# Kernel tuning notes

Hardware: AMD Instinct MI355X
Metric: run time of the kernel (lower is better)

## Reference

```python
import jax, jax.numpy as jnp
import numpy as np

B, S, H, D = 256, 512, 512, 1  # batch, seq_len, rnn_hid_size (== S*D), input_dim


def lstm_cell(x, h, c, Wih, Whh, bih, bhh):
    # torch.nn.LSTMCell: gates ordered i, f, g, o
    g = x @ Wih.T + bih + h @ Whh.T + bhh  # [B, 4H]
    i, f, gg, o = jnp.split(g, 4, axis=-1)
    i = jax.nn.sigmoid(i)
    f = jax.nn.sigmoid(f)
    gg = jnp.tanh(gg)
    o = jax.nn.sigmoid(o)
    c_new = f * c + i * gg
    h_new = o * jnp.tanh(c_new)
    return h_new, c_new


def setup_inputs() -> dict:
    key = jax.random.key(0)
    ks = jax.random.split(key, 14)
    sc = 1.0 / np.sqrt(H)  # torch LSTMCell/Linear default uniform bound
    u = lambda k, shape: jax.random.uniform(k, shape, jnp.float32, -sc, sc)
    values = jax.random.normal(ks[0], (B, S), jnp.float32)
    masks = jax.random.randint(ks[1], (B, S), 0, 2).astype(jnp.float32)
    return {
        "values": values,
        "masks": masks,
        "Wih_f": u(ks[2], (4 * H, D)), "Whh_f": u(ks[3], (4 * H, H)),
        "bih_f": u(ks[4], (4 * H,)), "bhh_f": u(ks[5], (4 * H,)),
        "Wih_b": u(ks[6], (4 * H, D)), "Whh_b": u(ks[7], (4 * H, H)),
        "bih_b": u(ks[8], (4 * H,)), "bhh_b": u(ks[9], (4 * H,)),
        "W_imp": u(ks[10], (D, H)), "b_imp": u(ks[11], (D,)),
    }


def reference(values, masks, Wih_f, Whh_f, bih_f, bhh_f,
              Wih_b, Whh_b, bih_b, bhh_b, W_imp, b_imp):
    x_f = values[:, :, None]  # [B, S, 1]
    m_f = masks[:, :, None]
    # flip over axis 2 (size 1) is a no-op, matching the original exactly
    x_b = jnp.flip(x_f, axis=2)
    m_b = jnp.flip(m_f, axis=2)

    start_f = jnp.full((B, D), 128.0, jnp.float32)
    start_b = jnp.full((B, D), -128.0, jnp.float32)
    z = jnp.zeros((B, H), jnp.float32)
    h_f, c_f = lstm_cell(start_f, z, z, Wih_f, Whh_f, bih_f, bhh_f)
    h_b, c_b = lstm_cell(start_b, z, z, Wih_b, Whh_b, bih_b, bhh_b)

    xs = (jnp.swapaxes(x_f, 0, 1), jnp.swapaxes(m_f, 0, 1),
          jnp.swapaxes(x_b, 0, 1), jnp.swapaxes(m_b, 0, 1))  # [S, B, 1] each

    def step(carry, inp):
        hf, cf, hb, cb = carry
        xf, mf, xb, mb = inp
        imp_f = hf @ W_imp.T + b_imp
        imp_b = hb @ W_imp.T + b_imp
        cc_f = (1.0 - mf) * xf + mf * imp_f
        cc_b = (1.0 - mb) * xb + mb * imp_b
        hf, cf = lstm_cell(cc_f, hf, cf, Wih_f, Whh_f, bih_f, bhh_f)
        hb, cb = lstm_cell(cc_b, hb, cb, Wih_b, Whh_b, bih_b, bhh_b)
        return (hf, cf, hb, cb), None

    (h_f, c_f, h_b, c_b), _ = jax.lax.scan(step, (h_f, c_f, h_b, c_b), xs)
    h = h_f + h_b  # [B, H]
    imputations = h.reshape(B, S, D)  # requires H == S * D
    out = imputations * (1.0 - m_f) + x_f * m_f
    return h, out
```

## Files before the change

### kernel.cpp

```cpp
#include <hip/hip_runtime.h>
#include <stdint.h>

#define B_ 256
#define S_ 512
#define H_ 512

#define XM_STRIDE 513
#define LDS_BYTES 56320

typedef __attribute__((ext_vector_type(4))) float f32x4;
typedef __attribute__((ext_vector_type(4))) int   i32x4;
typedef __attribute__((ext_vector_type(8))) short s16x8;

__device__ __forceinline__ short f2bf(float f) {
    union { float f; uint32_t u; } c; c.f = f;
    uint32_t u = c.u;
    u += 0x7fffu + ((u >> 16) & 1u);
    return (short)(u >> 16);
}
__device__ __forceinline__ float bflo(uint32_t u) { return __builtin_bit_cast(float, u << 16); }
__device__ __forceinline__ float bfhi(uint32_t u) { return __builtin_bit_cast(float, u & 0xffff0000u); }
__device__ __forceinline__ float sig_(float x)  { return 1.0f / (1.0f + __expf(-x)); }
__device__ __forceinline__ float tanh_(float x) { return 1.0f - 2.0f / (1.0f + __expf(2.0f * x)); }

__device__ __forceinline__ void load_a16_issue(const void* p, i32x4* a) {
    asm volatile(
        "global_load_dwordx4 %0, %16, off sc0 sc1\n\t"
        "global_load_dwordx4 %1, %16, off offset:64 sc0 sc1\n\t"
        "global_load_dwordx4 %2, %16, off offset:128 sc0 sc1\n\t"
        "global_load_dwordx4 %3, %16, off offset:192 sc0 sc1\n\t"
        "global_load_dwordx4 %4, %16, off offset:256 sc0 sc1\n\t"
        "global_load_dwordx4 %5, %16, off offset:320 sc0 sc1\n\t"
        "global_load_dwordx4 %6, %16, off offset:384 sc0 sc1\n\t"
        "global_load_dwordx4 %7, %16, off offset:448 sc0 sc1\n\t"
        "global_load_dwordx4 %8, %16, off offset:512 sc0 sc1\n\t"
        "global_load_dwordx4 %9, %16, off offset:576 sc0 sc1\n\t"
        "global_load_dwordx4 %10, %16, off offset:640 sc0 sc1\n\t"
        "global_load_dwordx4 %11, %16, off offset:704 sc0 sc1\n\t"
        "global_load_dwordx4 %12, %16, off offset:768 sc0 sc1\n\t"
        "global_load_dwordx4 %13, %16, off offset:832 sc0 sc1\n\t"
        "global_load_dwordx4 %14, %16, off offset:896 sc0 sc1\n\t"
        "global_load_dwordx4 %15, %16, off offset:960 sc0 sc1"
        : "=v"(a[0]), "=v"(a[1]), "=v"(a[2]), "=v"(a[3]),
          "=v"(a[4]), "=v"(a[5]), "=v"(a[6]), "=v"(a[7]),
          "=v"(a[8]), "=v"(a[9]), "=v"(a[10]), "=v"(a[11]),
          "=v"(a[12]), "=v"(a[13]), "=v"(a[14]), "=v"(a[15])
        : "v"(p)
        : "memory");
}
#define AWAIT(imm, x0, x1, x2, x3) \
    asm volatile("s_waitcnt vmcnt(" #imm ")" : "+v"(x0), "+v"(x1), "+v"(x2), "+v"(x3) :: "memory")

__device__ __forceinline__ void store_h4(void* p, int h0, int h1, int h2, int h3) {
    asm volatile(
        "global_store_short %4, %0, off sc0 sc1\n\t"
        "global_store_short %4, %1, off offset:1024 sc0 sc1\n\t"
        "global_store_short %4, %2, off offset:2048 sc0 sc1\n\t"
        "global_store_short %4, %3, off offset:3072 sc0 sc1"
        :: "v"(h0), "v"(h1), "v"(h2), "v"(h3), "v"(p)
        : "memory");
}

__global__ void __launch_bounds__(128, 1)
lstm_kernel(const float* __restrict__ values, const float* __restrict__ masks,
            const float* __restrict__ Wih_f, const float* __restrict__ Whh_f,
            const float* __restrict__ bih_f, const float* __restrict__ bhh_f,
            const float* __restrict__ Wih_b, const float* __restrict__ Whh_b,
            const float* __restrict__ bih_b, const float* __restrict__ bhh_b,
            const float* __restrict__ W_imp, const float* __restrict__ b_imp,
            unsigned int* ctrs, short* h_buf, float* hfin)
{
    extern __shared__ char smem_raw[];
    short*    imp_lds = (short*)smem_raw;
    uint32_t* xm_lds  = (uint32_t*)(smem_raw + 16384);

    uint32_t* flags = (uint32_t*)ctrs + 64;

    const int tid  = threadIdx.x;
    const int lane = tid & 63;
    const int wave = tid >> 6;
    const int nw = wave;

    const int bid = blockIdx.x;
    const int g   = bid & 15;
    const int w   = (bid >> 4) & 15;
    const int d   = bid >> 8;
    const int cluster = d * 16 + g;

    const float* Whh = d ? Whh_b : Whh_f;
    const float* Wih = d ? Wih_b : Wih_f;
    const float* bih = d ? bih_b : bih_f;
    const float* bhh = d ? bhh_b : bhh_f;

    const int col16 = lane & 15;
    const int koff4 = lane >> 4;
    const int jcol  = w * 32 + nw * 16 + col16;

    for (int c = tid; c < 1024; c += 128) {
        int ckoff = (c >> 4) & 3, ckb = c >> 6;
        int k0 = ckb * 32 + ckoff * 8;
        short* dst = &imp_lds[c * 8];
        #pragma unroll
        for (int j = 0; j < 8; ++j) dst[j] = f2bf(W_imp[k0 + j]);
    }
    for (int i = tid; i < 16 * 512; i += 128) {
        int r = i >> 9, s = i & 511;
        float x = values[(g * 16 + r) * S_ + s];
        float m = masks[(g * 16 + r) * S_ + s];
        float a = x * (1.0f - m);
        xm_lds[r * XM_STRIDE + s] =
            (uint32_t)(uint16_t)f2bf(a) | ((uint32_t)(uint16_t)f2bf(m) << 16);
    }

    s16x8 bfr[4][16];
    {
        const float* base = Whh + (size_t)jcol * 512 + koff4 * 8;
        #pragma unroll
        for (int gg = 0; gg < 4; ++gg) {
            const float* src = base + (size_t)gg * 512 * 512;
            #pragma unroll
            for (int kb = 0; kb < 16; ++kb) {
                f32x4 v0 = *(const f32x4*)(src + kb * 32);
                f32x4 v1 = *(const f32x4*)(src + kb * 32 + 4);
                s16x8 b;
                b[0] = f2bf(v0[0]); b[1] = f2bf(v0[1]); b[2] = f2bf(v0[2]); b[3] = f2bf(v0[3]);
                b[4] = f2bf(v1[0]); b[5] = f2bf(v1[1]); b[6] = f2bf(v1[2]); b[7] = f2bf(v1[3]);
                bfr[gg][kb] = b;
            }
        }
    }

    float bias[4], wih[4];
    #pragma unroll
    for (int gg = 0; gg < 4; ++gg) {
        int gc = gg * 512 + jcol;
        bias[gg] = bih[gc] + bhh[gc];
        wih[gg]  = Wih[gc];
    }
    const float bimp  = b_imp[0];
    const float start = d ? -128.0f : 128.0f;

    const int arow    = g * 16 + col16;
    const int rowloc  = koff4 * 4;
    const int rowbase = g * 16 + rowloc;
    const int imp_off = (koff4 * 16 + col16) * 8;

    uint32_t*       myflag = flags + cluster * 16 + w;
    const uint32_t* pollp  = flags + cluster * 16 + col16;

    __syncthreads();

    float c_reg[4];
    {
        float pre[4];
        #pragma unroll
        for (int gg = 0; gg < 4; ++gg) pre[gg] = start * wih[gg] + bias[gg];
        float i0 = sig_(pre[0]), g0 = tanh_(pre[2]), o0 = sig_(pre[3]);
        float c0 = i0 * g0;
        float h0 = o0 * tanh_(c0);
        #pragma unroll
        for (int r = 0; r < 4; ++r) c_reg[r] = c0;
        int hb16 = (int)(unsigned short)(unsigned)f2bf(h0);
        short* dst = h_buf + d * (B_ * H_) + (size_t)rowbase * H_ + jcol;
        store_h4(dst, hb16, hb16, hb16, hb16);
    }
    asm volatile("s_waitcnt vmcnt(0)" ::: "memory");
    __syncthreads();
    if (tid == 0)
        asm volatile("global_store_dword %0, %1, off sc0 sc1" :: "v"(myflag), "v"(1u) : "memory");

    for (int t = 0; t < S_; ++t) {
        const int p = t & 1;
        const short* hb_r = h_buf + p       * (2 * B_ * H_) + d * (B_ * H_);
        short*       hb_w = h_buf + (p ^ 1) * (2 * B_ * H_) + d * (B_ * H_);

        if (wave == 0) {
            const uint32_t tgt = (uint32_t)(t + 1);
            for (;;) {
                uint32_t f;
                asm volatile("global_load_dword %0, %1, off sc0 sc1\n\ts_waitcnt vmcnt(0)"
                             : "=v"(f) : "v"(pollp) : "memory");
                if (__ballot(f >= tgt) == ~0ull) break;
                __builtin_amdgcn_s_sleep(2);
            }
        }
        __syncthreads();

        i32x4 a_regs[16];
        load_a16_issue(hb_r + (size_t)arow * H_ + koff4 * 8, a_regs);

        f32x4 acc0 = {0,0,0,0}, acc1 = {0,0,0,0}, acc2 = {0,0,0,0}, acc3 = {0,0,0,0};
        f32x4 acc4 = {0,0,0,0};
        AWAIT(12, a_regs[0], a_regs[1], a_regs[2], a_regs[3]);
        #pragma unroll
        for (int kb = 0; kb < 4; ++kb) {
            s16x8 a = __builtin_bit_cast(s16x8, a_regs[kb]);
            acc0 = __builtin_amdgcn_mfma_f32_16x16x32_bf16(a, bfr[0][kb], acc0, 0, 0, 0);
            acc1 = __builtin_amdgcn_mfma_f32_16x16x32_bf16(a, bfr[1][kb], acc1, 0, 0, 0);
            acc2 = __builtin_amdgcn_mfma_f32_16x16x32_bf16(a, bfr[2][kb], acc2, 0, 0, 0);
            acc3 = __builtin_amdgcn_mfma_f32_16x16x32_bf16(a, bfr[3][kb], acc3, 0, 0, 0);
            s16x8 b4 = *(const s16x8*)&imp_lds[kb * 512 + imp_off];
            acc4 = __builtin_amdgcn_mfma_f32_16x16x32_bf16(a, b4, acc4, 0, 0, 0);
        }
        AWAIT(8, a_regs[4], a_regs[5], a_regs[6], a_regs[7]);
        #pragma unroll
        for (int kb = 4; kb < 8; ++kb) {
            s16x8 a = __builtin_bit_cast(s16x8, a_regs[kb]);
            acc0 = __builtin_amdgcn_mfma_f32_16x16x32_bf16(a, bfr[0][kb], acc0, 0, 0, 0);
            acc1 = __builtin_amdgcn_mfma_f32_16x16x32_bf16(a, bfr[1][kb], acc1, 0, 0, 0);
            acc2 = __builtin_amdgcn_mfma_f32_16x16x32_bf16(a, bfr[2][kb], acc2, 0, 0, 0);
            acc3 = __builtin_amdgcn_mfma_f32_16x16x32_bf16(a, bfr[3][kb], acc3, 0, 0, 0);
            s16x8 b4 = *(const s16x8*)&imp_lds[kb * 512 + imp_off];
            acc4 = __builtin_amdgcn_mfma_f32_16x16x32_bf16(a, b4, acc4, 0, 0, 0);
        }
        AWAIT(4, a_regs[8], a_regs[9], a_regs[10], a_regs[11]);
        #pragma unroll
        for (int kb = 8; kb < 12; ++kb) {
            s16x8 a = __builtin_bit_cast(s16x8, a_regs[kb]);
            acc0 = __builtin_amdgcn_mfma_f32_16x16x32_bf16(a, bfr[0][kb], acc0, 0, 0, 0);
            acc1 = __builtin_amdgcn_mfma_f32_16x16x32_bf16(a, bfr[1][kb], acc1, 0, 0, 0);
            acc2 = __builtin_amdgcn_mfma_f32_16x16x32_bf16(a, bfr[2][kb], acc2, 0, 0, 0);
            acc3 = __builtin_amdgcn_mfma_f32_16x16x32_bf16(a, bfr[3][kb], acc3, 0, 0, 0);
            s16x8 b4 = *(const s16x8*)&imp_lds[kb * 512 + imp_off];
            acc4 = __builtin_amdgcn_mfma_f32_16x16x32_bf16(a, b4, acc4, 0, 0, 0);
        }
        AWAIT(0, a_regs[12], a_regs[13], a_regs[14], a_regs[15]);
        #pragma unroll
        for (int kb = 12; kb < 16; ++kb) {
            s16x8 a = __builtin_bit_cast(s16x8, a_regs[kb]);
            acc0 = __builtin_amdgcn_mfma_f32_16x16x32_bf16(a, bfr[0][kb], acc0, 0, 0, 0);
            acc1 = __builtin_amdgcn_mfma_f32_16x16x32_bf16(a, bfr[1][kb], acc1, 0, 0, 0);
            acc2 = __builtin_amdgcn_mfma_f32_16x16x32_bf16(a, bfr[2][kb], acc2, 0, 0, 0);
            acc3 = __builtin_amdgcn_mfma_f32_16x16x32_bf16(a, bfr[3][kb], acc3, 0, 0, 0);
            s16x8 b4 = *(const s16x8*)&imp_lds[kb * 512 + imp_off];
            acc4 = __builtin_amdgcn_mfma_f32_16x16x32_bf16(a, b4, acc4, 0, 0, 0);
        }

        int hbits[4];
        #pragma unroll
        for (int r = 0; r < 4; ++r) {
            uint32_t pk = xm_lds[(rowloc + r) * XM_STRIDE + t];
            float cc = bflo(pk) + bfhi(pk) * (acc4[r] + bimp);
            float pi = acc0[r] + cc * wih[0] + bias[0];
            float pf = acc1[r] + cc * wih[1] + bias[1];
            float pg = acc2[r] + cc * wih[2] + bias[2];
            float po = acc3[r] + cc * wih[3] + bias[3];
            float iv = sig_(pi), fv = sig_(pf), gv = tanh_(pg), ov = sig_(po);
            c_reg[r] = fv * c_reg[r] + iv * gv;
            float hn = ov * tanh_(c_reg[r]);
            hbits[r] = (int)(unsigned short)(unsigned)f2bf(hn);
            if (t == S_ - 1) hfin[d * (B_ * H_) + (rowbase + r) * H_ + jcol] = hn;
        }
        store_h4(hb_w + (size_t)rowbase * H_ + jcol, hbits[0], hbits[1], hbits[2], hbits[3]);

        asm volatile("s_waitcnt vmcnt(0)" ::: "memory");
        __syncthreads();
        if (tid == 0)
            asm volatile("global_store_dword %0, %1, off sc0 sc1"
                         :: "v"(myflag), "v"((uint32_t)(t + 2)) : "memory");
    }
}

__global__ void __launch_bounds__(256)
epilogue_kernel(const float* __restrict__ values, const float* __restrict__ masks,
                const float* __restrict__ hfin, float* __restrict__ out)
{
    int i = blockIdx.x * 256 + threadIdx.x;
    float h = hfin[i] + hfin[B_ * H_ + i];
    out[i] = h;
    float xv = values[i], mv = masks[i];
    out[B_ * H_ + i] = h * (1.0f - mv) + xv * mv;
}

extern "C" void kernel_launch(void* const* d_in, const int* in_sizes, int n_in,
                              void* d_out, int out_size, void* d_ws, size_t ws_size,
                              hipStream_t stream) {
    const float* values = (const float*)d_in[0];
    const float* masks  = (const float*)d_in[1];
    const float* Wih_f  = (const float*)d_in[2];
    const float* Whh_f  = (const float*)d_in[3];
    const float* bih_f  = (const float*)d_in[4];
    const float* bhh_f  = (const float*)d_in[5];
    const float* Wih_b  = (const float*)d_in[6];
    const float* Whh_b  = (const float*)d_in[7];
    const float* bih_b  = (const float*)d_in[8];
    const float* bhh_b  = (const float*)d_in[9];
    const float* W_imp  = (const float*)d_in[10];
    const float* b_imp  = (const float*)d_in[11];

    unsigned int* ctrs = (unsigned int*)d_ws;
    short* h_buf = (short*)((char*)d_ws + 8192);
    float* hfin  = (float*)((char*)d_ws + 8192 + 2 * 2 * B_ * H_ * sizeof(short));

    hipMemsetAsync(d_ws, 0, 8192, stream);

    hipFuncSetAttribute((const void*)lstm_kernel,
                        hipFuncAttributeMaxDynamicSharedMemorySize, LDS_BYTES);

    void* args[] = {
        (void*)&values, (void*)&masks,
        (void*)&Wih_f, (void*)&Whh_f, (void*)&bih_f, (void*)&bhh_f,
        (void*)&Wih_b, (void*)&Whh_b, (void*)&bih_b, (void*)&bhh_b,
        (void*)&W_imp, (void*)&b_imp,
        (void*)&ctrs, (void*)&h_buf, (void*)&hfin
    };
    hipError_t err = hipLaunchCooperativeKernel((const void*)lstm_kernel,
                                                dim3(512), dim3(128), args,
                                                (unsigned int)LDS_BYTES, stream);
    if (err != hipSuccess) {
        lstm_kernel<<<dim3(512), dim3(128), LDS_BYTES, stream>>>(
            values, masks, Wih_f, Whh_f, bih_f, bhh_f,
            Wih_b, Whh_b, bih_b, bhh_b, W_imp, b_imp, ctrs, h_buf, hfin);
    }

    epilogue_kernel<<<dim3((B_ * H_) / 256), dim3(256), 0, stream>>>(
        values, masks, hfin, (float*)d_out);
}
```

Measured before the change: 2.309 ms.

## Replace flag-based inter-block sync with sentinel polling on a 4-deep h ring

Drops the per-step flag counters, block barriers and store fences. Each block now polls the hidden-state data itself, retrying the load until no lane sees the 0xAAAA sentinel, and resets a stale ring slot back to the sentinel after each step. This is meant to remove one global round trip plus barrier latency from every recurrent step. It also writes the final h straight into the output buffer instead of a scratch buffer. Risks: repeated full-tile reloads while polling add memory traffic, the staged waits that overlapped loads with MFMA are gone, and a genuine bf16 value equal to the sentinel would stall the loop.

```diff
diff --git a/kernel.cpp b/kernel.cpp
--- a/kernel.cpp
+++ b/kernel.cpp
@@ -7,6 +7,8 @@
 
 #define XM_STRIDE 513
 #define LDS_BYTES 56320
+
+#define SENT ((int)0xAAAAAAAA)
 
 typedef __attribute__((ext_vector_type(4))) float f32x4;
 typedef __attribute__((ext_vector_type(4))) int   i32x4;
@@ -23,7 +25,7 @@
 __device__ __forceinline__ float sig_(float x)  { return 1.0f / (1.0f + __expf(-x)); }
 __device__ __forceinline__ float tanh_(float x) { return 1.0f - 2.0f / (1.0f + __expf(2.0f * x)); }
 
-__device__ __forceinline__ void load_a16_issue(const void* p, i32x4* a) {
+__device__ __forceinline__ void load_a16(const void* p, i32x4* a) {
     asm volatile(
         "global_load_dwordx4 %0, %16, off sc0 sc1\n\t"
         "global_load_dwordx4 %1, %16, off offset:64 sc0 sc1\n\t"
@@ -40,7 +42,8 @@
         "global_load_dwordx4 %12, %16, off offset:768 sc0 sc1\n\t"
         "global_load_dwordx4 %13, %16, off offset:832 sc0 sc1\n\t"
         "global_load_dwordx4 %14, %16, off offset:896 sc0 sc1\n\t"
-        "global_load_dwordx4 %15, %16, off offset:960 sc0 sc1"
+        "global_load_dwordx4 %15, %16, off offset:960 sc0 sc1\n\t"
+        "s_waitcnt vmcnt(0)"
         : "=v"(a[0]), "=v"(a[1]), "=v"(a[2]), "=v"(a[3]),
           "=v"(a[4]), "=v"(a[5]), "=v"(a[6]), "=v"(a[7]),
           "=v"(a[8]), "=v"(a[9]), "=v"(a[10]), "=v"(a[11]),
@@ -48,8 +51,6 @@
         : "v"(p)
         : "memory");
 }
-#define AWAIT(imm, x0, x1, x2, x3) \
-    asm volatile("s_waitcnt vmcnt(" #imm ")" : "+v"(x0), "+v"(x1), "+v"(x2), "+v"(x3) :: "memory")
 
 __device__ __forceinline__ void store_h4(void* p, int h0, int h1, int h2, int h3) {
     asm volatile(
@@ -68,24 +69,21 @@
             const float* __restrict__ Wih_b, const float* __restrict__ Whh_b,
             const float* __restrict__ bih_b, const float* __restrict__ bhh_b,
             const float* __restrict__ W_imp, const float* __restrict__ b_imp,
-            unsigned int* ctrs, short* h_buf, float* hfin)
+            short* h_buf, float* outbuf)
 {
     extern __shared__ char smem_raw[];
     short*    imp_lds = (short*)smem_raw;
     uint32_t* xm_lds  = (uint32_t*)(smem_raw + 16384);
 
-    uint32_t* flags = (uint32_t*)ctrs + 64;
-
     const int tid  = threadIdx.x;
     const int lane = tid & 63;
-    const int wave = tid >> 6;
-    const int nw = wave;
+    const int nw   = tid >> 6;
 
     const int bid = blockIdx.x;
     const int g   = bid & 15;
     const int w   = (bid >> 4) & 15;
     const int d   = bid >> 8;
-    const int cluster = d * 16 + g;
+    const int dofs = d * (B_ * H_);
 
     const float* Whh = d ? Whh_b : Whh_f;
     const float* Wih = d ? Wih_b : Wih_f;
@@ -145,9 +143,6 @@
     const int rowbase = g * 16 + rowloc;
     const int imp_off = (koff4 * 16 + col16) * 8;
 
-    uint32_t*       myflag = flags + cluster * 16 + w;
-    const uint32_t* pollp  = flags + cluster * 16 + col16;
-
     __syncthreads();
 
     float c_reg[4];
@@ -161,72 +156,36 @@
         #pragma unroll
         for (int r = 0; r < 4; ++r) c_reg[r] = c0;
         int hb16 = (int)(unsigned short)(unsigned)f2bf(h0);
-        short* dst = h_buf + d * (B_ * H_) + (size_t)rowbase * H_ + jcol;
-        store_h4(dst, hb16, hb16, hb16, hb16);
-    }
-    asm volatile("s_waitcnt vmcnt(0)" ::: "memory");
-    __syncthreads();
-    if (tid == 0)
-        asm volatile("global_store_dword %0, %1, off sc0 sc1" :: "v"(myflag), "v"(1u) : "memory");
-
+        store_h4(h_buf + dofs + (size_t)rowbase * H_ + jcol, hb16, hb16, hb16, hb16);
+    }
+
+    const size_t lane_off = (size_t)rowbase * H_ + jcol;
+    const size_t aoff     = (size_t)arow * H_ + koff4 * 8;
     for (int t = 0; t < S_; ++t) {
-        const int p = t & 1;
-        const short* hb_r = h_buf + p       * (2 * B_ * H_) + d * (B_ * H_);
-        short*       hb_w = h_buf + (p ^ 1) * (2 * B_ * H_) + d * (B_ * H_);
-
-        if (wave == 0) {
-            const uint32_t tgt = (uint32_t)(t + 1);
+        const short* rbuf = h_buf + ((t)     & 3) * (2 * B_ * H_) + dofs;
+        short*       wbuf = h_buf + ((t + 1) & 3) * (2 * B_ * H_) + dofs;
+        short*       sbuf = h_buf + ((t + 3) & 3) * (2 * B_ * H_) + dofs;
+
+        i32x4 a_regs[16];
+        {
+            const void* ap = rbuf + aoff;
             for (;;) {
-                uint32_t f;
-                asm volatile("global_load_dword %0, %1, off sc0 sc1\n\ts_waitcnt vmcnt(0)"
-                             : "=v"(f) : "v"(pollp) : "memory");
-                if (__ballot(f >= tgt) == ~0ull) break;
-                __builtin_amdgcn_s_sleep(2);
+                load_a16(ap, a_regs);
+                int bad = 0;
+                #pragma unroll
+                for (int j = 0; j < 16; ++j) {
+                    i32x4 v = a_regs[j];
+                    bad |= (v[0] == SENT) | (v[1] == SENT) | (v[2] == SENT) | (v[3] == SENT);
+                }
+                if (__ballot(bad != 0) == 0ull) break;
+                __builtin_amdgcn_s_sleep(1);
             }
         }
-        __syncthreads();
-
-        i32x4 a_regs[16];
-        load_a16_issue(hb_r + (size_t)arow * H_ + koff4 * 8, a_regs);
 
         f32x4 acc0 = {0,0,0,0}, acc1 = {0,0,0,0}, acc2 = {0,0,0,0}, acc3 = {0,0,0,0};
         f32x4 acc4 = {0,0,0,0};
-        AWAIT(12, a_regs[0], a_regs[1], a_regs[2], a_regs[3]);
-        #pragma unroll
-        for (int kb = 0; kb < 4; ++kb) {
-            s16x8 a = __builtin_bit_cast(s16x8, a_regs[kb]);
-            acc0 = __builtin_amdgcn_mfma_f32_16x16x32_bf16(a, bfr[0][kb], acc0, 0, 0, 0);
-            acc1 = __builtin_amdgcn_mfma_f32_16x16x32_bf16(a, bfr[1][kb], acc1, 0, 0, 0);
-            acc2 = __builtin_amdgcn_mfma_f32_16x16x32_bf16(a, bfr[2][kb], acc2, 0, 0, 0);
-            acc3 = __builtin_amdgcn_mfma_f32_16x16x32_bf16(a, bfr[3][kb], acc3, 0, 0, 0);
-            s16x8 b4 = *(const s16x8*)&imp_lds[kb * 512 + imp_off];
-            acc4 = __builtin_amdgcn_mfma_f32_16x16x32_bf16(a, b4, acc4, 0, 0, 0);
-        }
-        AWAIT(8, a_regs[4], a_regs[5], a_regs[6], a_regs[7]);
-        #pragma unroll
-        for (int kb = 4; kb < 8; ++kb) {
-            s16x8 a = __builtin_bit_cast(s16x8, a_regs[kb]);
-            acc0 = __builtin_amdgcn_mfma_f32_16x16x32_bf16(a, bfr[0][kb], acc0, 0, 0, 0);
-            acc1 = __builtin_amdgcn_mfma_f32_16x16x32_bf16(a, bfr[1][kb], acc1, 0, 0, 0);
-            acc2 = __builtin_amdgcn_mfma_f32_16x16x32_bf16(a, bfr[2][kb], acc2, 0, 0, 0);
-            acc3 = __builtin_amdgcn_mfma_f32_16x16x32_bf16(a, bfr[3][kb], acc3, 0, 0, 0);
-            s16x8 b4 = *(const s16x8*)&imp_lds[kb * 512 + imp_off];
-            acc4 = __builtin_amdgcn_mfma_f32_16x16x32_bf16(a, b4, acc4, 0, 0, 0);
-        }
-        AWAIT(4, a_regs[8], a_regs[9], a_regs[10], a_regs[11]);
-        #pragma unroll
-        for (int kb = 8; kb < 12; ++kb) {
-            s16x8 a = __builtin_bit_cast(s16x8, a_regs[kb]);
-            acc0 = __builtin_amdgcn_mfma_f32_16x16x32_bf16(a, bfr[0][kb], acc0, 0, 0, 0);
-            acc1 = __builtin_amdgcn_mfma_f32_16x16x32_bf16(a, bfr[1][kb], acc1, 0, 0, 0);
-            acc2 = __builtin_amdgcn_mfma_f32_16x16x32_bf16(a, bfr[2][kb], acc2, 0, 0, 0);
-            acc3 = __builtin_amdgcn_mfma_f32_16x16x32_bf16(a, bfr[3][kb], acc3, 0, 0, 0);
-            s16x8 b4 = *(const s16x8*)&imp_lds[kb * 512 + imp_off];
-            acc4 = __builtin_amdgcn_mfma_f32_16x16x32_bf16(a, b4, acc4, 0, 0, 0);
-        }
-        AWAIT(0, a_regs[12], a_regs[13], a_regs[14], a_regs[15]);
-        #pragma unroll
-        for (int kb = 12; kb < 16; ++kb) {
+        #pragma unroll
+        for (int kb = 0; kb < 16; ++kb) {
             s16x8 a = __builtin_bit_cast(s16x8, a_regs[kb]);
             acc0 = __builtin_amdgcn_mfma_f32_16x16x32_bf16(a, bfr[0][kb], acc0, 0, 0, 0);
             acc1 = __builtin_amdgcn_mfma_f32_16x16x32_bf16(a, bfr[1][kb], acc1, 0, 0, 0);
@@ -249,24 +208,20 @@
             c_reg[r] = fv * c_reg[r] + iv * gv;
             float hn = ov * tanh_(c_reg[r]);
             hbits[r] = (int)(unsigned short)(unsigned)f2bf(hn);
-            if (t == S_ - 1) hfin[d * (B_ * H_) + (rowbase + r) * H_ + jcol] = hn;
-        }
-        store_h4(hb_w + (size_t)rowbase * H_ + jcol, hbits[0], hbits[1], hbits[2], hbits[3]);
-
-        asm volatile("s_waitcnt vmcnt(0)" ::: "memory");
-        __syncthreads();
-        if (tid == 0)
-            asm volatile("global_store_dword %0, %1, off sc0 sc1"
-                         :: "v"(myflag), "v"((uint32_t)(t + 2)) : "memory");
+            if (t == S_ - 1) outbuf[dofs + lane_off + (size_t)r * H_] = hn;
+        }
+        store_h4(wbuf + lane_off, hbits[0], hbits[1], hbits[2], hbits[3]);
+        store_h4(sbuf + lane_off, 0xAAAA, 0xAAAA, 0xAAAA, 0xAAAA);
     }
 }
 
 __global__ void __launch_bounds__(256)
 epilogue_kernel(const float* __restrict__ values, const float* __restrict__ masks,
-                const float* __restrict__ hfin, float* __restrict__ out)
+                float* __restrict__ out)
 {
     int i = blockIdx.x * 256 + threadIdx.x;
-    float h = hfin[i] + hfin[B_ * H_ + i];
+    float hf = out[i], hb = out[B_ * H_ + i];
+    float h = hf + hb;
     out[i] = h;
     float xv = values[i], mv = masks[i];
     out[B_ * H_ + i] = h * (1.0f - mv) + xv * mv;
@@ -288,11 +243,10 @@
     const float* W_imp  = (const float*)d_in[10];
     const float* b_imp  = (const float*)d_in[11];
 
-    unsigned int* ctrs = (unsigned int*)d_ws;
-    short* h_buf = (short*)((char*)d_ws + 8192);
-    float* hfin  = (float*)((char*)d_ws + 8192 + 2 * 2 * B_ * H_ * sizeof(short));
-
-    hipMemsetAsync(d_ws, 0, 8192, stream);
+    short* h_buf = (short*)d_ws;
+    hipMemsetAsync(d_ws, 0xAA, 4 * 2 * B_ * H_ * sizeof(short), stream);
+
+    float* outbuf = (float*)d_out;
 
     hipFuncSetAttribute((const void*)lstm_kernel,
                         hipFuncAttributeMaxDynamicSharedMemorySize, LDS_BYTES);
@@ -302,7 +256,7 @@
         (void*)&Wih_f, (void*)&Whh_f, (void*)&bih_f, (void*)&bhh_f,
         (void*)&Wih_b, (void*)&Whh_b, (void*)&bih_b, (void*)&bhh_b,
         (void*)&W_imp, (void*)&b_imp,
-        (void*)&ctrs, (void*)&h_buf, (void*)&hfin
+        (void*)&h_buf, (void*)&outbuf
     };
     hipError_t err = hipLaunchCooperativeKernel((const void*)lstm_kernel,
                                                 dim3(512), dim3(128), args,
@@ -310,9 +264,9 @@
     if (err != hipSuccess) {
         lstm_kernel<<<dim3(512), dim3(128), LDS_BYTES, stream>>>(
             values, masks, Wih_f, Whh_f, bih_f, bhh_f,
-            Wih_b, Whh_b, bih_b, bhh_b, W_imp, b_imp, ctrs, h_buf, hfin);
+            Wih_b, Whh_b, bih_b, bhh_b, W_imp, b_imp, h_buf, outbuf);
     }
 
     epilogue_kernel<<<dim3((B_ * H_) / 256), dim3(256), 0, stream>>>(
-        values, masks, hfin, (float*)d_out);
-}
+        values, masks, outbuf);
+}
```

After: 4.910 ms. 113% more time.

## Use per-wave step flags and LDS-transposed coalesced hidden-state stores

Applied to the files above, without the earlier changes.

Each wave now publishes its own step-completion flag, so the block-wide barrier before signalling is gone. Consumers poll 32 flags per cluster instead of 16, which needs a larger flag region and memset. The scattered 2-byte global stores of h are replaced by a small per-wave LDS transpose followed by one dwordx2 store per lane, and the spin-wait sleep is shortened. The aim is lower per-timestep latency on the serial recurrence, paid for with more flag polling traffic and an extra LDS round trip.

```diff
diff --git a/kernel.cpp b/kernel.cpp
--- a/kernel.cpp
+++ b/kernel.cpp
@@ -10,6 +10,7 @@
 
 typedef __attribute__((ext_vector_type(4))) float f32x4;
 typedef __attribute__((ext_vector_type(4))) int   i32x4;
+typedef __attribute__((ext_vector_type(2))) int   i32x2;
 typedef __attribute__((ext_vector_type(8))) short s16x8;
 
 __device__ __forceinline__ short f2bf(float f) {
@@ -73,13 +74,13 @@
     extern __shared__ char smem_raw[];
     short*    imp_lds = (short*)smem_raw;
     uint32_t* xm_lds  = (uint32_t*)(smem_raw + 16384);
+    short*    tr_lds  = (short*)(smem_raw + 49216);
 
     uint32_t* flags = (uint32_t*)ctrs + 64;
 
     const int tid  = threadIdx.x;
     const int lane = tid & 63;
-    const int wave = tid >> 6;
-    const int nw = wave;
+    const int nw   = tid >> 6;
 
     const int bid = blockIdx.x;
     const int g   = bid & 15;
@@ -145,8 +146,12 @@
     const int rowbase = g * 16 + rowloc;
     const int imp_off = (koff4 * 16 + col16) * 8;
 
-    uint32_t*       myflag = flags + cluster * 16 + w;
-    const uint32_t* pollp  = flags + cluster * 16 + col16;
+    uint32_t*       myflag = flags + cluster * 64 + w * 2 + nw;
+    const uint32_t* pollp  = flags + cluster * 64 + (lane & 31);
+
+    short* trw = tr_lds + nw * 320;
+    const int row16 = lane & 15;
+    const int half  = lane >> 4;
 
     __syncthreads();
 
@@ -161,12 +166,10 @@
         #pragma unroll
         for (int r = 0; r < 4; ++r) c_reg[r] = c0;
         int hb16 = (int)(unsigned short)(unsigned)f2bf(h0);
-        short* dst = h_buf + d * (B_ * H_) + (size_t)rowbase * H_ + jcol;
-        store_h4(dst, hb16, hb16, hb16, hb16);
+        store_h4(h_buf + d * (B_ * H_) + (size_t)rowbase * H_ + jcol, hb16, hb16, hb16, hb16);
     }
     asm volatile("s_waitcnt vmcnt(0)" ::: "memory");
-    __syncthreads();
-    if (tid == 0)
+    if (lane == 0)
         asm volatile("global_store_dword %0, %1, off sc0 sc1" :: "v"(myflag), "v"(1u) : "memory");
 
     for (int t = 0; t < S_; ++t) {
@@ -174,14 +177,14 @@
         const short* hb_r = h_buf + p       * (2 * B_ * H_) + d * (B_ * H_);
         short*       hb_w = h_buf + (p ^ 1) * (2 * B_ * H_) + d * (B_ * H_);
 
-        if (wave == 0) {
+        if (nw == 0) {
             const uint32_t tgt = (uint32_t)(t + 1);
             for (;;) {
                 uint32_t f;
                 asm volatile("global_load_dword %0, %1, off sc0 sc1\n\ts_waitcnt vmcnt(0)"
                              : "=v"(f) : "v"(pollp) : "memory");
                 if (__ballot(f >= tgt) == ~0ull) break;
-                __builtin_amdgcn_s_sleep(2);
+                __builtin_amdgcn_s_sleep(1);
             }
         }
         __syncthreads();
@@ -249,13 +252,20 @@
             c_reg[r] = fv * c_reg[r] + iv * gv;
             float hn = ov * tanh_(c_reg[r]);
             hbits[r] = (int)(unsigned short)(unsigned)f2bf(hn);
-            if (t == S_ - 1) hfin[d * (B_ * H_) + (rowbase + r) * H_ + jcol] = hn;
-        }
-        store_h4(hb_w + (size_t)rowbase * H_ + jcol, hbits[0], hbits[1], hbits[2], hbits[3]);
+            if (t == S_ - 1)
+                hfin[d * (B_ * H_) + (size_t)(rowbase + r) * H_ + jcol] = hn;
+        }
+
+        #pragma unroll
+        for (int r = 0; r < 4; ++r)
+            trw[(rowloc + r) * 20 + col16] = (short)hbits[r];
+        asm volatile("s_waitcnt lgkmcnt(0)" ::: "memory");
+        i32x2 hv = *(const i32x2*)&trw[row16 * 20 + half * 4];
+        short* dstp = hb_w + (size_t)(g * 16 + row16) * H_ + w * 32 + nw * 16 + half * 4;
+        asm volatile("global_store_dwordx2 %0, %1, off sc0 sc1" :: "v"(dstp), "v"(hv) : "memory");
 
         asm volatile("s_waitcnt vmcnt(0)" ::: "memory");
-        __syncthreads();
-        if (tid == 0)
+        if (lane == 0)
             asm volatile("global_store_dword %0, %1, off sc0 sc1"
                          :: "v"(myflag), "v"((uint32_t)(t + 2)) : "memory");
     }
@@ -289,10 +299,10 @@
     const float* b_imp  = (const float*)d_in[11];
 
     unsigned int* ctrs = (unsigned int*)d_ws;
-    short* h_buf = (short*)((char*)d_ws + 8192);
-    float* hfin  = (float*)((char*)d_ws + 8192 + 2 * 2 * B_ * H_ * sizeof(short));
-
-    hipMemsetAsync(d_ws, 0, 8192, stream);
+    short* h_buf = (short*)((char*)d_ws + 16384);
+    float* hfin  = (float*)((char*)d_ws + 16384 + 2 * 2 * B_ * H_ * sizeof(short));
+
+    hipMemsetAsync(d_ws, 0, 16384, stream);
 
     hipFuncSetAttribute((const void*)lstm_kernel,
                         hipFuncAttributeMaxDynamicSharedMemorySize, LDS_BYTES);
```

Result: slower. 2.447 ms (+6.0%).
